# Kernel tuning notes

Measured on AMD Instinct MI355X. Metric: run time of the kernel, lower is better.

## Reference

```python
import jax, jax.numpy as jnp
import numpy as np

N_STEPS = 128  # window length (matches init_kwargs n_steps)
N = 8_388_608  # sequence length


def setup_inputs() -> dict:
    key = jax.random.key(0)
    x = jax.random.normal(key, (N,), dtype=jnp.float32)
    return {"input_attenuation": x}


def reference(input_attenuation):
    # Causal sliding-window min: out[i] = min(x[max(0, i-N_STEPS+1) : i+1]).
    # Left-pad with +inf (identity of min) so early positions use shorter windows,
    # then a single fused reduce_window replaces the O(N) Python loop.
    pad = jnp.full((N_STEPS - 1,), jnp.inf, dtype=input_attenuation.dtype)
    xp = jnp.concatenate([pad, input_attenuation])  # [N + N_STEPS - 1]
    out = jax.lax.reduce_window(
        xp,
        jnp.inf,
        jax.lax.min,
        window_dimensions=(N_STEPS,),
        window_strides=(1,),
        padding="VALID",
    )  # [N]
    return out
```

## Files before the change

### kernel.cpp

```cpp
#include <hip/hip_runtime.h>
#include <math.h>

#define WAVE 64
#define E    16
#define SPAN (WAVE * E)
#define W    128
#define OUTS (SPAN - W)

__global__ __launch_bounds__(256) void swmin_kernel(const float* __restrict__ x,
                                                    float* __restrict__ out,
                                                    int n) {
    const int wave_id = blockIdx.x * (blockDim.x / WAVE) + (threadIdx.x / WAVE);
    const int lane    = threadIdx.x & (WAVE - 1);
    const int base    = wave_id * OUTS - W;
    const int lbase   = base + lane * E;

    float b[E];

#pragma unroll
    for (int k = 0; k < E / 4; ++k) {
        const int p = lbase + 4 * k;
        if (p >= 0 && p + 3 < n) {
            const float4 v = *reinterpret_cast<const float4*>(x + p);
            b[4 * k + 0] = v.x; b[4 * k + 1] = v.y;
            b[4 * k + 2] = v.z; b[4 * k + 3] = v.w;
        } else {
            b[4 * k + 0] = INFINITY; b[4 * k + 1] = INFINITY;
            b[4 * k + 2] = INFINITY; b[4 * k + 3] = INFINITY;
        }
    }

#pragma unroll
    for (int s = 1; s < E; s <<= 1) {
        float t[E];
#pragma unroll
        for (int j = 0; j < s; ++j)
            t[j] = __shfl_up(b[E - s + j], 1);
#pragma unroll
        for (int j = E - 1; j >= s; --j)
            b[j] = fminf(b[j], b[j - s]);
#pragma unroll
        for (int j = 0; j < s; ++j)
            b[j] = fminf(b[j], t[j]);
    }
#pragma unroll
    for (int s = E; s <= W / 2; s <<= 1) {
        const int L = s / E;
        float t[E];
#pragma unroll
        for (int j = 0; j < E; ++j)
            t[j] = __shfl_up(b[j], L);
#pragma unroll
        for (int j = 0; j < E; ++j)
            b[j] = fminf(b[j], t[j]);
    }

    if (lane >= W / E) {
#pragma unroll
        for (int k = 0; k < E / 4; ++k) {
            const int p = lbase + 4 * k;
            if (p + 3 < n) {
                *reinterpret_cast<float4*>(out + p) =
                    make_float4(b[4 * k + 0], b[4 * k + 1], b[4 * k + 2], b[4 * k + 3]);
            }
        }
    }
}

extern "C" void kernel_launch(void* const* d_in, const int* in_sizes, int n_in,
                              void* d_out, int out_size, void* d_ws, size_t ws_size,
                              hipStream_t stream) {
    const float* x = (const float*)d_in[0];
    float* out     = (float*)d_out;
    const int n    = in_sizes[0];

    const int waves_per_block = 256 / WAVE;
    const int total_waves     = (n + OUTS - 1) / OUTS;
    const int blocks          = (total_waves + waves_per_block - 1) / waves_per_block;

    swmin_kernel<<<blocks, 256, 0, stream>>>(x, out, n);
}
```

Measured before the change: 88.46 us.

## Replace shuffle-heavy scan with block prefix/suffix (van Herk) sliding-window min

Replaces the log-step wave-wide min scan over every element with a block decomposition: each lane computes local prefix and suffix mins, small 8-lane group scans produce cross-lane prefix/suffix, and each output combines a block prefix with the previous block's suffix fetched by one shuffle per element. This cuts the number of cross-lane shuffles and min operations per element. It adds register pressure for separate prefix, suffix and result arrays.

```diff
diff --git a/kernel.cpp b/kernel.cpp
--- a/kernel.cpp
+++ b/kernel.cpp
@@ -6,62 +6,74 @@
 #define SPAN (WAVE * E)
 #define W    128
 #define OUTS (SPAN - W)
+#define GL   (W / E)
 
 __global__ __launch_bounds__(256) void swmin_kernel(const float* __restrict__ x,
                                                     float* __restrict__ out,
                                                     int n) {
     const int wave_id = blockIdx.x * (blockDim.x / WAVE) + (threadIdx.x / WAVE);
     const int lane    = threadIdx.x & (WAVE - 1);
-    const int base    = wave_id * OUTS - W;
-    const int lbase   = base + lane * E;
+    const int g       = lane & (GL - 1);
+    const int lbase   = wave_id * OUTS - W + lane * E;
 
-    float b[E];
-
+    float v[E];
 #pragma unroll
     for (int k = 0; k < E / 4; ++k) {
-        const int p = lbase + 4 * k;
-        if (p >= 0 && p + 3 < n) {
-            const float4 v = *reinterpret_cast<const float4*>(x + p);
-            b[4 * k + 0] = v.x; b[4 * k + 1] = v.y;
-            b[4 * k + 2] = v.z; b[4 * k + 3] = v.w;
+        const int pos = lbase + 4 * k;
+        if (pos >= 0 && pos + 3 < n) {
+            const float4 f = *reinterpret_cast<const float4*>(x + pos);
+            v[4 * k + 0] = f.x; v[4 * k + 1] = f.y;
+            v[4 * k + 2] = f.z; v[4 * k + 3] = f.w;
         } else {
-            b[4 * k + 0] = INFINITY; b[4 * k + 1] = INFINITY;
-            b[4 * k + 2] = INFINITY; b[4 * k + 3] = INFINITY;
+            v[4 * k + 0] = INFINITY; v[4 * k + 1] = INFINITY;
+            v[4 * k + 2] = INFINITY; v[4 * k + 3] = INFINITY;
         }
     }
 
+    float p[E], s[E];
+    p[0] = v[0];
 #pragma unroll
-    for (int s = 1; s < E; s <<= 1) {
-        float t[E];
+    for (int j = 1; j < E; ++j) p[j] = fminf(p[j - 1], v[j]);
+    s[E - 1] = v[E - 1];
 #pragma unroll
-        for (int j = 0; j < s; ++j)
-            t[j] = __shfl_up(b[E - s + j], 1);
+    for (int j = E - 2; j >= 0; --j) s[j] = fminf(s[j + 1], v[j]);
+    const float tot = p[E - 1];
+
+    float a = tot;
+    {
+        float t = __shfl_up(a, 1); if (g >= 1) a = fminf(a, t);
+        t       = __shfl_up(a, 2); if (g >= 2) a = fminf(a, t);
+        t       = __shfl_up(a, 4); if (g >= 4) a = fminf(a, t);
+    }
+    float t0 = __shfl_up(a, 1);
+    const float Epre = (g >= 1) ? t0 : INFINITY;
+
+    float b = tot;
+    {
+        float t = __shfl_down(b, 1); if (g + 1 <= GL - 1) b = fminf(b, t);
+        t       = __shfl_down(b, 2); if (g + 2 <= GL - 1) b = fminf(b, t);
+        t       = __shfl_down(b, 4); if (g + 4 <= GL - 1) b = fminf(b, t);
+    }
+    float t1 = __shfl_down(b, 1);
+    const float Esuf = (g <= GL - 2) ? t1 : INFINITY;
+
+    float R[E];
 #pragma unroll
-        for (int j = E - 1; j >= s; --j)
-            b[j] = fminf(b[j], b[j - s]);
-#pragma unroll
-        for (int j = 0; j < s; ++j)
-            b[j] = fminf(b[j], t[j]);
-    }
-#pragma unroll
-    for (int s = E; s <= W / 2; s <<= 1) {
-        const int L = s / E;
-        float t[E];
-#pragma unroll
-        for (int j = 0; j < E; ++j)
-            t[j] = __shfl_up(b[j], L);
-#pragma unroll
-        for (int j = 0; j < E; ++j)
-            b[j] = fminf(b[j], t[j]);
-    }
+    for (int j = 0; j < E - 1; ++j)
+        R[j] = __shfl_up(fminf(Esuf, s[j + 1]), GL);
+    R[E - 1] = __shfl_up(fminf(Esuf, s[0]), GL - 1);
 
-    if (lane >= W / E) {
+    if (lane >= GL) {
 #pragma unroll
         for (int k = 0; k < E / 4; ++k) {
-            const int p = lbase + 4 * k;
-            if (p + 3 < n) {
-                *reinterpret_cast<float4*>(out + p) =
-                    make_float4(b[4 * k + 0], b[4 * k + 1], b[4 * k + 2], b[4 * k + 3]);
+            const int pos = lbase + 4 * k;
+            if (pos + 3 < n) {
+                float4 o;
+                o.x = fminf(fminf(Epre, p[4 * k + 0]), R[4 * k + 0]);
+                o.y = fminf(fminf(Epre, p[4 * k + 1]), R[4 * k + 1]);
+                o.z = fminf(fminf(Epre, p[4 * k + 2]), R[4 * k + 2]);
+                o.w = fminf(fminf(Epre, p[4 * k + 3]), R[4 * k + 3]);
+                *reinterpret_cast<float4*>(out + pos) = o;
             }
         }
     }
```

Measured after the change: 88.59 us. About the same (+0.1%).
